# Performance work log

Hardware: AMD Instinct MI355X
Metric: run time of the kernel (lower is better)

## Reference

```python
import jax, jax.numpy as jnp
import numpy as np

THR1 = 0.8     # lif1 threshold
THR2 = 1.0     # lif2 (Synaptic) default threshold
ALPHA2 = 0.9   # Synaptic alpha (not learnable, use_stdp=False)
BETA2 = 0.8    # Synaptic beta
SLOPE = 25.0   # snntorch fast_sigmoid default slope

@jax.custom_vjp
def fast_sigmoid_spike(x):
    return (x > 0).astype(x.dtype)

def _fs_fwd(x):
    return fast_sigmoid_spike(x), x

def _fs_bwd(x, g):
    return (g / (SLOPE * jnp.abs(x) + 1.0) ** 2,)

fast_sigmoid_spike.defvjp(_fs_fwd, _fs_bwd)

@jax.custom_vjp
def atan_spike(x):  # snntorch default ATan surrogate, alpha=2.0
    return (x > 0).astype(x.dtype)

def _at_fwd(x):
    return atan_spike(x), x

def _at_bwd(x, g):
    return (g / (1.0 + (jnp.pi * x) ** 2),)

atan_spike.defvjp(_at_fwd, _at_bwd)

def setup_inputs() -> dict:
    key = jax.random.key(0)
    k = jax.random.split(key, 6)
    B, S, V, H, E, T = 16, 16, 16000, 512, 256, 20
    x = jax.random.randint(k[0], (B, S), 0, V)
    embed_w = jax.random.normal(k[1], (V, E), dtype=jnp.float32)  # torch Embedding ~ N(0,1)
    fc1_w = jax.random.normal(k[2], (H, E), dtype=jnp.float32) / np.sqrt(E)
    fc1_b = jax.random.normal(k[3], (H,), dtype=jnp.float32) / np.sqrt(E)
    fc2_w = jax.random.normal(k[4], (V, H), dtype=jnp.float32) / np.sqrt(H)
    fc2_b = jax.random.normal(k[5], (V,), dtype=jnp.float32) / np.sqrt(H)
    beta1 = jnp.float32(0.85)  # learnable Leaky beta
    return {"x": x, "embed_w": embed_w, "fc1_w": fc1_w, "fc1_b": fc1_b,
            "fc2_w": fc2_w, "fc2_b": fc2_b, "beta1": beta1, "time_steps": T}

def reference(x, embed_w, fc1_w, fc1_b, fc2_w, fc2_b, beta1, time_steps):
    B, S = x.shape
    H = fc1_w.shape[0]
    V = fc2_w.shape[0]
    emb = embed_w[x]                       # [B, S, 256]
    b1 = jnp.clip(beta1, 0.0, 1.0)
    mem1 = jnp.zeros((B, H), emb.dtype)
    syn2 = jnp.zeros((B, V), emb.dtype)
    mem2 = jnp.zeros((B, V), emb.dtype)

    def token_step(carry, emb_t):          # emb_t: [B, 256]
        mem1, syn2, mem2 = carry
        cur1 = emb_t @ fc1_w.T + fc1_b     # identical every inner step (hoisted)

        def inner(c, _):
            m1, s2, m2, _ = c
            reset = fast_sigmoid_spike(m1 - THR1)          # reset from previous mem
            m1 = b1 * m1 + cur1 - reset * THR1             # Leaky, subtract reset
            spk1 = fast_sigmoid_spike(m1 - THR1)
            cur2 = spk1 @ fc2_w.T + fc2_b                  # [B, V]
            s2 = ALPHA2 * s2 + cur2                        # Synaptic, reset='none'
            m2 = BETA2 * m2 + s2
            spk2 = atan_spike(m2 - THR2)
            return (m1, s2, m2, spk2), None

        (mem1, syn2, mem2, spk2), _ = jax.lax.scan(
            inner, (mem1, syn2, mem2, jnp.zeros_like(mem2)), None, length=time_steps)
        return (mem1, syn2, mem2), spk2    # keep last spk2 of inner loop

    (mem1, syn2, mem2), outs = jax.lax.scan(
        token_step, (mem1, syn2, mem2), jnp.swapaxes(emb, 0, 1))  # scan over seq
    out = jnp.transpose(outs, (1, 0, 2))   # [B, S, V]
    return out, mem1, syn2, mem2
```

## Files before the change

### kernel.cpp

```cpp
#include <hip/hip_runtime.h>

#define Bdim 16
#define Sdim 16
#define Edim 256
#define Hdim 512
#define Vdim 16000
#define THR1f 0.8f
#define THR2f 1.0f

typedef unsigned int   u32;
typedef unsigned short u16;
typedef __attribute__((ext_vector_type(8))) short bf16x8;
typedef __attribute__((ext_vector_type(4))) float f32x4;
typedef __attribute__((ext_vector_type(4))) u32   u32x4;

__device__ __forceinline__ u16 f2bf(float f) {
  u32 u = __float_as_uint(f);
  return (u16)((u + 0x7FFFu + ((u >> 16) & 1u)) >> 16);
}
__device__ __forceinline__ u32 pack2(float a, float b) {
  return (u32)f2bf(a) | ((u32)f2bf(b) << 16);
}

__global__ __launch_bounds__(256) void snn_prep(
    const int* __restrict__ x, const float* __restrict__ embed_w,
    const float* __restrict__ fc1_w, const float* __restrict__ fc1_b,
    const float* __restrict__ beta1p, const int* __restrict__ tsp,
    u16* __restrict__ Ab3, float* __restrict__ mem1)
{
  __shared__ __align__(16) float As[64][68];
  __shared__ __align__(16) float Ws[64][68];
  __shared__ float cbuf[64][68];
  __shared__ int sidx[64];
  const int tid = threadIdx.x;
  const int n0  = blockIdx.x * 64;
  const int bi0 = blockIdx.y * 4;
  const int tx = tid & 15, ty = tid >> 4;

  if (tid < 64) sidx[tid] = x[(bi0 + (tid & 3)) * Sdim + (tid >> 2)];

  float acc[4][4] = {{0.f}};
  for (int k0 = 0; k0 < Edim; k0 += 64) {
    __syncthreads();
#pragma unroll
    for (int i = 0; i < 16; ++i) {
      const int k = tid + i * 256;
      const int rr = k >> 6, j = k & 63;
      As[j][rr] = embed_w[(size_t)sidx[rr] * Edim + k0 + j];
      Ws[j][rr] = fc1_w[(size_t)(n0 + rr) * Edim + k0 + j];
    }
    __syncthreads();
#pragma unroll
    for (int j = 0; j < 64; ++j) {
      const float4 av = *(const float4*)&As[j][ty * 4];
      const float4 wv = *(const float4*)&Ws[j][tx * 4];
      const float a[4] = {av.x, av.y, av.z, av.w};
      const float w[4] = {wv.x, wv.y, wv.z, wv.w};
#pragma unroll
      for (int i = 0; i < 4; ++i)
#pragma unroll
        for (int jj = 0; jj < 4; ++jj)
          acc[i][jj] = fmaf(a[i], w[jj], acc[i][jj]);
    }
  }
#pragma unroll
  for (int i = 0; i < 4; ++i)
#pragma unroll
    for (int jj = 0; jj < 4; ++jj)
      cbuf[ty * 4 + i][tx * 4 + jj] = acc[i][jj] + fc1_b[n0 + tx * 4 + jj];
  __syncthreads();

  const int bb = tid >> 6, hl = tid & 63;
  const int b  = bi0 + bb;
  const int hg = n0 + hl;
  const float b1 = fminf(fmaxf(beta1p[0], 0.f), 1.f);
  const int T = tsp[0];

  double w9T = 1.0, w8T = 1.0;
  for (int i = 0; i < T; ++i) { w9T *= 0.9; w8T *= 0.8; }

  const int S = hg >> 5, q = (hg >> 3) & 3, jc = hg & 7;

  float m1 = 0.f;
  for (int t = 0; t < Sdim; ++t) {
    const float cur = cbuf[t * 4 + bb][hl];
    double p9 = w9T, p8 = w8T;
    float cs = 0.f, cm = 0.f;
    for (int u = 0; u < T; ++u) {
      const float reset = (m1 > THR1f) ? THR1f : 0.f;
      m1 = b1 * m1 + cur - reset;
      if (m1 > THR1f) {
        cs += (float)(p9 * (10.0 / 9.0));
        cm += (float)(10.0 * (p9 - p8));
      }
      p9 *= (10.0 / 9.0);
      p8 *= 1.25;
    }
    int rb = 2 * b;
    int R  = 2 * t + (rb >> 4);
    int l  = q * 16 + (rb & 15);
    Ab3[((size_t)(S * 32 + R) * 64 + l) * 8 + jc] = f2bf(cs);
    rb = 2 * b + 1;
    R  = 2 * t + (rb >> 4);
    l  = q * 16 + (rb & 15);
    Ab3[((size_t)(S * 32 + R) * 64 + l) * 8 + jc] = f2bf(cm);
  }
  mem1[b * Hdim + hg] = m1;
}

__global__ __launch_bounds__(256, 1) void snn_fused(
    const u16* __restrict__ Ab3, const float* __restrict__ W,
    const float* __restrict__ fc2_b, const int* __restrict__ tsp,
    float* __restrict__ out, float* __restrict__ syn2, float* __restrict__ mem2)
{
  const int tid  = threadIdx.x;
  const int lane = tid & 63;
  const int wn   = tid >> 6;
  const int v0   = blockIdx.x * 64;
  const int v    = v0 + wn * 16 + (lane & 15);

  f32x4 acc[32];
#pragma unroll
  for (int R = 0; R < 32; ++R)
#pragma unroll
    for (int e = 0; e < 4; ++e) acc[R][e] = 0.f;

  const float* wrow = W + (size_t)v * Hdim + ((lane >> 4) * 8);
  float4 wa = *(const float4*)(wrow);
  float4 wb = *(const float4*)(wrow + 4);

  for (int S = 0; S < 16; ++S) {
    const int Sn = (S + 1) & 15;
    const float4 na = *(const float4*)(wrow + Sn * 32);
    const float4 nb = *(const float4*)(wrow + Sn * 32 + 4);
    u32x4 bw;
    bw.x = pack2(wa.x, wa.y); bw.y = pack2(wa.z, wa.w);
    bw.z = pack2(wb.x, wb.y); bw.w = pack2(wb.z, wb.w);
    const bf16x8 bfr = __builtin_bit_cast(bf16x8, bw);
    const char* abase = (const char*)Ab3 + (size_t)S * 32768 + lane * 16;
#pragma unroll
    for (int R = 0; R < 32; ++R) {
      const bf16x8 af = *(const bf16x8*)(abase + R * 1024);
      acc[R] = __builtin_amdgcn_mfma_f32_16x16x32_bf16(af, bfr, acc[R],
                                                       0, 0, 0);
    }
    wa = na; wb = nb;
  }

  const int T = tsp[0];
  double p9 = 1.0, p8 = 1.0;
  for (int i = 0; i < T; ++i) { p9 *= 0.9; p8 *= 0.8; }
  const float Ps  = (float)p9;
  const float Pm  = (float)p8;
  const float Pms = (float)(0.9 * 10.0 * (p9 - p8));
  const float Sws = (float)(10.0 * (1.0 - p9));
  const float Swm = (float)(10.0 * (9.0 * (1.0 - p9) - 4.0 * (1.0 - p8)));

  const int g = lane >> 4;
  const float bbv = fc2_b[v];
  const float bbs = bbv * Sws;
  const float bbm = bbv * Swm;

#pragma unroll
  for (int hi = 0; hi < 2; ++hi) {
#pragma unroll
    for (int j = 0; j < 2; ++j) {
      const int b = hi * 8 + 2 * g + j;
      float s2 = 0.f, m2 = 0.f;
#pragma unroll
      for (int t = 0; t < Sdim; ++t) {
        const float gs = acc[2 * t + hi][2 * j];
        const float gm = acc[2 * t + hi][2 * j + 1];
        const float m2n = Pm * m2 + Pms * s2 + gm + bbm;
        s2 = Ps * s2 + gs + bbs;
        m2 = m2n;
        out[((size_t)b * Sdim + t) * Vdim + v] = (m2n > THR2f) ? 1.f : 0.f;
      }
      syn2[(size_t)b * Vdim + v] = s2;
      mem2[(size_t)b * Vdim + v] = m2;
    }
  }
}

extern "C" void kernel_launch(void* const* d_in, const int* in_sizes, int n_in,
                              void* d_out, int out_size, void* d_ws, size_t ws_size,
                              hipStream_t stream) {
  const int*   x       = (const int*)d_in[0];
  const float* embed_w = (const float*)d_in[1];
  const float* fc1_w   = (const float*)d_in[2];
  const float* fc1_b   = (const float*)d_in[3];
  const float* fc2_w   = (const float*)d_in[4];
  const float* fc2_b   = (const float*)d_in[5];
  const float* beta1   = (const float*)d_in[6];
  const int*   tsteps  = (const int*)d_in[7];

  float* out  = (float*)d_out;
  float* mem1 = out + (size_t)Bdim * Sdim * Vdim;
  float* syn2 = mem1 + (size_t)Bdim * Hdim;
  float* mem2 = syn2 + (size_t)Bdim * Vdim;

  u16* Ab3 = (u16*)d_ws;

  snn_prep<<<dim3(8, 4), 256, 0, stream>>>(x, embed_w, fc1_w, fc1_b,
                                           beta1, tsteps, Ab3, mem1);
  snn_fused<<<Vdim / 64, 256, 0, stream>>>(Ab3, fc2_w, fc2_b, tsteps,
                                           out, syn2, mem2);
}
```

Before: 174.9 us.

## Split K across two waves per block with LDS reduction and double-buffered A loads

The fused kernel now gives each block 16 vocab columns and two waves. Each wave handles half of the hidden (K) dimension, and the partial MFMA accumulators are reduced through shared memory before the recurrence epilogue. A-fragment loads are double-buffered in groups of 8 so they overlap the MFMAs. This raises the block count fourfold (1000 blocks) for better latency hiding and occupancy. In exchange it adds a 32KB LDS reduction, extra syncs, and more total reads of the Ab3 tile across blocks.

```diff
diff --git a/kernel.cpp b/kernel.cpp
--- a/kernel.cpp
+++ b/kernel.cpp
@@ -108,16 +108,19 @@
   mem1[b * Hdim + hg] = m1;
 }
 
-__global__ __launch_bounds__(256, 1) void snn_fused(
+__global__ __launch_bounds__(128, 2) void snn_fused(
     const u16* __restrict__ Ab3, const float* __restrict__ W,
     const float* __restrict__ fc2_b, const int* __restrict__ tsp,
     float* __restrict__ out, float* __restrict__ syn2, float* __restrict__ mem2)
 {
+  __shared__ __align__(16) float red[32][64][4];
   const int tid  = threadIdx.x;
   const int lane = tid & 63;
-  const int wn   = tid >> 6;
-  const int v0   = blockIdx.x * 64;
-  const int v    = v0 + wn * 16 + (lane & 15);
+  const int w    = tid >> 6;
+  const int v0   = blockIdx.x * 16;
+  const int col  = lane & 15;
+  const int grp  = lane >> 4;
+  const int v    = v0 + col;
 
   f32x4 acc[32];
 #pragma unroll
@@ -125,27 +128,61 @@
 #pragma unroll
     for (int e = 0; e < 4; ++e) acc[R][e] = 0.f;
 
-  const float* wrow = W + (size_t)v * Hdim + ((lane >> 4) * 8);
-  float4 wa = *(const float4*)(wrow);
-  float4 wb = *(const float4*)(wrow + 4);
-
-  for (int S = 0; S < 16; ++S) {
-    const int Sn = (S + 1) & 15;
-    const float4 na = *(const float4*)(wrow + Sn * 32);
-    const float4 nb = *(const float4*)(wrow + Sn * 32 + 4);
+  const float* wrow = W + (size_t)v * Hdim + grp * 8;
+  float4 wa = *(const float4*)(wrow + (8 * w) * 32);
+  float4 wb = *(const float4*)(wrow + (8 * w) * 32 + 4);
+
+  for (int s = 0; s < 8; ++s) {
+    const int S  = 8 * w + s;
+    const int sn = (s < 7) ? s + 1 : 7;
+    const float4 na = *(const float4*)(wrow + (8 * w + sn) * 32);
+    const float4 nb = *(const float4*)(wrow + (8 * w + sn) * 32 + 4);
+
     u32x4 bw;
     bw.x = pack2(wa.x, wa.y); bw.y = pack2(wa.z, wa.w);
     bw.z = pack2(wb.x, wb.y); bw.w = pack2(wb.z, wb.w);
     const bf16x8 bfr = __builtin_bit_cast(bf16x8, bw);
+
     const char* abase = (const char*)Ab3 + (size_t)S * 32768 + lane * 16;
-#pragma unroll
-    for (int R = 0; R < 32; ++R) {
-      const bf16x8 af = *(const bf16x8*)(abase + R * 1024);
-      acc[R] = __builtin_amdgcn_mfma_f32_16x16x32_bf16(af, bfr, acc[R],
-                                                       0, 0, 0);
+    bf16x8 af[8], ag[8];
+#pragma unroll
+    for (int i = 0; i < 8; ++i)
+      af[i] = *(const bf16x8*)(abase + i * 1024);
+#pragma unroll
+    for (int gof = 0; gof < 4; ++gof) {
+      bf16x8* curb = (gof & 1) ? ag : af;
+      bf16x8* nxtb = (gof & 1) ? af : ag;
+      if (gof < 3) {
+#pragma unroll
+        for (int i = 0; i < 8; ++i)
+          nxtb[i] = *(const bf16x8*)(abase + ((gof + 1) * 8 + i) * 1024);
+      }
+#pragma unroll
+      for (int i = 0; i < 8; ++i)
+        acc[gof * 8 + i] = __builtin_amdgcn_mfma_f32_16x16x32_bf16(
+            curb[i], bfr, acc[gof * 8 + i], 0, 0, 0);
     }
     wa = na; wb = nb;
   }
+
+  if (w == 1) {
+#pragma unroll
+    for (int R = 0; R < 32; ++R)
+      *(f32x4*)&red[R][lane][0] = acc[R];
+  }
+  __syncthreads();
+  if (w == 0) {
+#pragma unroll
+    for (int R = 0; R < 32; ++R)
+      acc[R] += *(const f32x4*)&red[R][lane][0];
+  }
+  __syncthreads();
+  if (w == 0) {
+#pragma unroll
+    for (int R = 0; R < 32; ++R)
+      *(f32x4*)&red[R][lane][0] = acc[R];
+  }
+  __syncthreads();
 
   const int T = tsp[0];
   double p9 = 1.0, p8 = 1.0;
@@ -156,29 +193,27 @@
   const float Sws = (float)(10.0 * (1.0 - p9));
   const float Swm = (float)(10.0 * (9.0 * (1.0 - p9) - 4.0 * (1.0 - p8)));
 
-  const int g = lane >> 4;
   const float bbv = fc2_b[v];
   const float bbs = bbv * Sws;
   const float bbm = bbv * Swm;
 
 #pragma unroll
-  for (int hi = 0; hi < 2; ++hi) {
-#pragma unroll
-    for (int j = 0; j < 2; ++j) {
-      const int b = hi * 8 + 2 * g + j;
-      float s2 = 0.f, m2 = 0.f;
-#pragma unroll
-      for (int t = 0; t < Sdim; ++t) {
-        const float gs = acc[2 * t + hi][2 * j];
-        const float gm = acc[2 * t + hi][2 * j + 1];
-        const float m2n = Pm * m2 + Pms * s2 + gm + bbm;
-        s2 = Ps * s2 + gs + bbs;
-        m2 = m2n;
-        out[((size_t)b * Sdim + t) * Vdim + v] = (m2n > THR2f) ? 1.f : 0.f;
-      }
-      syn2[(size_t)b * Vdim + v] = s2;
-      mem2[(size_t)b * Vdim + v] = m2;
-    }
+  for (int jj = 0; jj < 2; ++jj) {
+    const int b = w * 8 + grp * 2 + jj;
+    float s2 = 0.f, m2 = 0.f;
+#pragma unroll
+    for (int t = 0; t < Sdim; ++t) {
+      const int rs = 32 * t + 2 * b;
+      const float gs = red[rs >> 4][((rs & 15) >> 2) * 16 + col][rs & 3];
+      const int rm = rs + 1;
+      const float gm = red[rm >> 4][((rm & 15) >> 2) * 16 + col][rm & 3];
+      const float m2n = Pm * m2 + Pms * s2 + gm + bbm;
+      s2 = Ps * s2 + gs + bbs;
+      m2 = m2n;
+      out[((size_t)b * Sdim + t) * Vdim + v] = (m2n > THR2f) ? 1.f : 0.f;
+    }
+    syn2[(size_t)b * Vdim + v] = s2;
+    mem2[(size_t)b * Vdim + v] = m2;
   }
 }
 
@@ -203,6 +238,6 @@
 
   snn_prep<<<dim3(8, 4), 256, 0, stream>>>(x, embed_w, fc1_w, fc1_b,
                                            beta1, tsteps, Ab3, mem1);
-  snn_fused<<<Vdim / 64, 256, 0, stream>>>(Ab3, fc2_w, fc2_b, tsteps,
+  snn_fused<<<Vdim / 16, 128, 0, stream>>>(Ab3, fc2_w, fc2_b, tsteps,
                                            out, syn2, mem2);
 }
```

New measurement: 155.2 us. 11.3% less time.

## Split fused GEMM across 8 waves by row tiles with serialized scan via LDS

Applied to the files above, without the earlier changes.

The fused kernel now uses 512 threads, and each of its 8 waves owns 4 of the 32 row tiles (2 timesteps) across all 64 output columns, where before each of 4 waves held 32 accumulators. Both the A fragments and the W rows are double-buffered in registers to overlap loads with MFMAs. The syn2/mem2 recurrence is then chained across waves in order through LDS, with a __syncthreads between each of the 8 stages. This cuts register pressure and raises occupancy, but it serializes the epilogue across waves and makes every wave convert the full W tile to bf16 redundantly.

```diff
diff --git a/kernel.cpp b/kernel.cpp
--- a/kernel.cpp
+++ b/kernel.cpp
@@ -108,43 +108,76 @@
   mem1[b * Hdim + hg] = m1;
 }
 
-__global__ __launch_bounds__(256, 1) void snn_fused(
+__global__ __launch_bounds__(512, 2) void snn_fused(
     const u16* __restrict__ Ab3, const float* __restrict__ W,
     const float* __restrict__ fc2_b, const int* __restrict__ tsp,
     float* __restrict__ out, float* __restrict__ syn2, float* __restrict__ mem2)
 {
+  __shared__ float2 st[16][64];
   const int tid  = threadIdx.x;
   const int lane = tid & 63;
-  const int wn   = tid >> 6;
+  const int wr   = tid >> 6;
   const int v0   = blockIdx.x * 64;
-  const int v    = v0 + wn * 16 + (lane & 15);
-
-  f32x4 acc[32];
-#pragma unroll
-  for (int R = 0; R < 32; ++R)
-#pragma unroll
-    for (int e = 0; e < 4; ++e) acc[R][e] = 0.f;
-
-  const float* wrow = W + (size_t)v * Hdim + ((lane >> 4) * 8);
-  float4 wa = *(const float4*)(wrow);
-  float4 wb = *(const float4*)(wrow + 4);
-
+  const int col  = lane & 15;
+  const int grp  = lane >> 4;
+
+  f32x4 acc[4][4];
+#pragma unroll
+  for (int i = 0; i < 4; ++i)
+#pragma unroll
+    for (int c = 0; c < 4; ++c)
+#pragma unroll
+      for (int e = 0; e < 4; ++e) acc[i][c][e] = 0.f;
+
+  const char* abase = (const char*)Ab3 + (wr << 12) + lane * 16;
+  const float* wp0 = W + (size_t)(v0 + 0  + col) * Hdim + grp * 8;
+  const float* wp1 = W + (size_t)(v0 + 16 + col) * Hdim + grp * 8;
+  const float* wp2 = W + (size_t)(v0 + 32 + col) * Hdim + grp * 8;
+  const float* wp3 = W + (size_t)(v0 + 48 + col) * Hdim + grp * 8;
+
+  bf16x8 aBuf[2][4];
+  float4 wBuf[2][8];
+
+#pragma unroll
+  for (int i = 0; i < 4; ++i)
+    aBuf[0][i] = *(const bf16x8*)(abase + i * 1024);
+  wBuf[0][0] = *(const float4*)(wp0);     wBuf[0][1] = *(const float4*)(wp0 + 4);
+  wBuf[0][2] = *(const float4*)(wp1);     wBuf[0][3] = *(const float4*)(wp1 + 4);
+  wBuf[0][4] = *(const float4*)(wp2);     wBuf[0][5] = *(const float4*)(wp2 + 4);
+  wBuf[0][6] = *(const float4*)(wp3);     wBuf[0][7] = *(const float4*)(wp3 + 4);
+
+#pragma unroll
   for (int S = 0; S < 16; ++S) {
-    const int Sn = (S + 1) & 15;
-    const float4 na = *(const float4*)(wrow + Sn * 32);
-    const float4 nb = *(const float4*)(wrow + Sn * 32 + 4);
-    u32x4 bw;
-    bw.x = pack2(wa.x, wa.y); bw.y = pack2(wa.z, wa.w);
-    bw.z = pack2(wb.x, wb.y); bw.w = pack2(wb.z, wb.w);
-    const bf16x8 bfr = __builtin_bit_cast(bf16x8, bw);
-    const char* abase = (const char*)Ab3 + (size_t)S * 32768 + lane * 16;
-#pragma unroll
-    for (int R = 0; R < 32; ++R) {
-      const bf16x8 af = *(const bf16x8*)(abase + R * 1024);
-      acc[R] = __builtin_amdgcn_mfma_f32_16x16x32_bf16(af, bfr, acc[R],
-                                                       0, 0, 0);
-    }
-    wa = na; wb = nb;
+    const int cur = S & 1, nxt = cur ^ 1;
+    if (S < 15) {
+      const int o = (S + 1) * 32;
+#pragma unroll
+      for (int i = 0; i < 4; ++i)
+        aBuf[nxt][i] = *(const bf16x8*)(abase + (S + 1) * 32768 + i * 1024);
+      wBuf[nxt][0] = *(const float4*)(wp0 + o);
+      wBuf[nxt][1] = *(const float4*)(wp0 + o + 4);
+      wBuf[nxt][2] = *(const float4*)(wp1 + o);
+      wBuf[nxt][3] = *(const float4*)(wp1 + o + 4);
+      wBuf[nxt][4] = *(const float4*)(wp2 + o);
+      wBuf[nxt][5] = *(const float4*)(wp2 + o + 4);
+      wBuf[nxt][6] = *(const float4*)(wp3 + o);
+      wBuf[nxt][7] = *(const float4*)(wp3 + o + 4);
+    }
+    bf16x8 bfr[4];
+#pragma unroll
+    for (int c = 0; c < 4; ++c) {
+      const float4 a = wBuf[cur][2 * c], b = wBuf[cur][2 * c + 1];
+      u32x4 bw;
+      bw.x = pack2(a.x, a.y); bw.y = pack2(a.z, a.w);
+      bw.z = pack2(b.x, b.y); bw.w = pack2(b.z, b.w);
+      bfr[c] = __builtin_bit_cast(bf16x8, bw);
+    }
+#pragma unroll
+    for (int i = 0; i < 4; ++i)
+#pragma unroll
+      for (int c = 0; c < 4; ++c)
+        acc[i][c] = __builtin_amdgcn_mfma_f32_16x16x32_bf16(
+            aBuf[cur][i], bfr[c], acc[i][c], 0, 0, 0);
   }
 
   const int T = tsp[0];
@@ -156,29 +189,68 @@
   const float Sws = (float)(10.0 * (1.0 - p9));
   const float Swm = (float)(10.0 * (9.0 * (1.0 - p9) - 4.0 * (1.0 - p8)));
 
-  const int g = lane >> 4;
-  const float bbv = fc2_b[v];
-  const float bbs = bbv * Sws;
-  const float bbm = bbv * Swm;
-
-#pragma unroll
-  for (int hi = 0; hi < 2; ++hi) {
-#pragma unroll
-    for (int j = 0; j < 2; ++j) {
-      const int b = hi * 8 + 2 * g + j;
-      float s2 = 0.f, m2 = 0.f;
-#pragma unroll
-      for (int t = 0; t < Sdim; ++t) {
-        const float gs = acc[2 * t + hi][2 * j];
-        const float gm = acc[2 * t + hi][2 * j + 1];
-        const float m2n = Pm * m2 + Pms * s2 + gm + bbm;
-        s2 = Ps * s2 + gs + bbs;
-        m2 = m2n;
-        out[((size_t)b * Sdim + t) * Vdim + v] = (m2n > THR2f) ? 1.f : 0.f;
+  float bbs[4], bbm[4];
+#pragma unroll
+  for (int c = 0; c < 4; ++c) {
+    const float bb = fc2_b[v0 + c * 16 + col];
+    bbs[c] = bb * Sws;
+    bbm[c] = bb * Swm;
+  }
+
+  for (int s = 0; s < 8; ++s) {
+    if (wr == s) {
+      float s2[4][4], m2[4][4];
+#pragma unroll
+      for (int c = 0; c < 4; ++c)
+#pragma unroll
+        for (int hi = 0; hi < 2; ++hi)
+#pragma unroll
+          for (int j = 0; j < 2; ++j) {
+            const int b = 8 * hi + 2 * grp + j;
+            if (s > 0) {
+              const float2 v2 = st[b][c * 16 + col];
+              s2[c][hi * 2 + j] = v2.x; m2[c][hi * 2 + j] = v2.y;
+            } else {
+              s2[c][hi * 2 + j] = 0.f; m2[c][hi * 2 + j] = 0.f;
+            }
+          }
+#pragma unroll
+      for (int tt = 0; tt < 2; ++tt) {
+        const int t = 2 * s + tt;
+#pragma unroll
+        for (int c = 0; c < 4; ++c)
+#pragma unroll
+          for (int hi = 0; hi < 2; ++hi)
+#pragma unroll
+            for (int j = 0; j < 2; ++j) {
+              const int b  = 8 * hi + 2 * grp + j;
+              const int si = hi * 2 + j;
+              const float gs = acc[2 * tt + hi][c][2 * j];
+              const float gm = acc[2 * tt + hi][c][2 * j + 1];
+              const float m2n = Pm * m2[c][si] + Pms * s2[c][si] + gm + bbm[c];
+              s2[c][si] = Ps * s2[c][si] + gs + bbs[c];
+              m2[c][si] = m2n;
+              out[((size_t)b * Sdim + t) * Vdim + v0 + c * 16 + col] =
+                  (m2n > THR2f) ? 1.f : 0.f;
+            }
       }
-      syn2[(size_t)b * Vdim + v] = s2;
-      mem2[(size_t)b * Vdim + v] = m2;
-    }
+#pragma unroll
+      for (int c = 0; c < 4; ++c)
+#pragma unroll
+        for (int hi = 0; hi < 2; ++hi)
+#pragma unroll
+          for (int j = 0; j < 2; ++j) {
+            const int b  = 8 * hi + 2 * grp + j;
+            const int si = hi * 2 + j;
+            if (s < 7) {
+              st[b][c * 16 + col] = make_float2(s2[c][si], m2[c][si]);
+            } else {
+              syn2[(size_t)b * Vdim + v0 + c * 16 + col] = s2[c][si];
+              mem2[(size_t)b * Vdim + v0 + c * 16 + col] = m2[c][si];
+            }
+          }
+    }
+    __syncthreads();
   }
 }
 
@@ -203,6 +275,6 @@
 
   snn_prep<<<dim3(8, 4), 256, 0, stream>>>(x, embed_w, fc1_w, fc1_b,
                                            beta1, tsteps, Ab3, mem1);
-  snn_fused<<<Vdim / 64, 256, 0, stream>>>(Ab3, fc2_w, fc2_b, tsteps,
+  snn_fused<<<Vdim / 64, 512, 0, stream>>>(Ab3, fc2_w, fc2_b, tsteps,
                                            out, syn2, mem2);
 }
```

After: 169.2 us. 3.2% less time.
